# Kernel tuning notes

Measured on AMD Instinct MI355X. Metric: run time of the kernel, lower is better.

The kernel has to match this reference:

```python
import jax, jax.numpy as jnp
import numpy as np

B, C, N, M, K = 1, 64, 65536, 65536, 16
H, O = 64, 128  # mlp hidden, out_channels


def setup_inputs() -> dict:
    key = jax.random.key(0)
    ks = jax.random.split(key, 8)
    return {
        "x": jax.random.normal(ks[0], (B, C, N), dtype=jnp.float32),
        "pos": jax.random.normal(ks[1], (B, 3, N), dtype=jnp.float32),
        "support_points": jax.random.normal(ks[2], (B, 3, M), dtype=jnp.float32),
        "W1": jax.random.normal(ks[3], (H, C + 3), dtype=jnp.float32) * 0.05,
        "b1": jax.random.normal(ks[4], (H,), dtype=jnp.float32) * 0.05,
        "W2": jax.random.normal(ks[5], (O, H), dtype=jnp.float32) * 0.05,
        "b2": jax.random.normal(ks[6], (O,), dtype=jnp.float32) * 0.05,
        "indices": jax.random.randint(ks[7], (B, M, K), 0, N, dtype=jnp.int64),
    }


def _gather_points(t, indices):
    # t: [B, C, N], indices: [B, M, K] -> [B, C, M, K]
    b, c, n = t.shape
    m, k = indices.shape[1], indices.shape[2]
    idx = indices.reshape(b, 1, m * k)  # broadcasts over channel dim
    return jnp.take_along_axis(t, idx, axis=2).reshape(b, c, m, k)


def reference(x, pos, support_points, W1, b1, W2, b2, indices):
    # gather neighbor features and positions: [B, C, M, K], [B, 3, M, K]
    feats = _gather_points(x, indices)
    pts = _gather_points(pos, indices) - support_points[:, :, :, None]
    h = jnp.concatenate([feats, pts], axis=1)  # [B, C+3, M, K]
    # shared per-point MLP (1x1 Conv2d == channel contraction)
    h = jnp.einsum("oc,bcmk->bomk", W1, h) + b1[None, :, None, None]
    h = jax.nn.relu(h)
    h = jnp.einsum("oc,bcmk->bomk", W2, h) + b2[None, :, None, None]
    # max-pool over neighborhood K -> [B, O, M]
    return jnp.max(h, axis=3)
```

## Files before the change

### kernel.cpp

```cpp
#include <hip/hip_runtime.h>
#include <hip/hip_bf16.h>

#define NPTS 65536
#define MPTS 65536

typedef __attribute__((ext_vector_type(8))) short bf16x8;
typedef __attribute__((ext_vector_type(4))) float f32x4;

__device__ __forceinline__ float bflo(unsigned int u){ union{unsigned int i; float f;} v; v.i = u<<16; return v.f; }
__device__ __forceinline__ float bfhi(unsigned int u){ union{unsigned int i; float f;} v; v.i = u & 0xffff0000u; return v.f; }
__device__ __forceinline__ unsigned short f2bf(float f){
  union{float f; unsigned int i;} v; v.f=f;
  unsigned int r = v.i + 0x7fffu + ((v.i>>16)&1u);
  return (unsigned short)(r>>16);
}
__device__ __forceinline__ unsigned int pk2f(float a, float b){
  float2 tf; tf.x = a; tf.y = b;
  union { __hip_bfloat162 h; unsigned int u; } c;
  c.h = __float22bfloat162_rn(tf);
  return c.u;
}
__device__ __forceinline__ float swz16(float x){
  return __int_as_float(__builtin_amdgcn_ds_swizzle(__float_as_int(x), 0x401F));
}
__device__ __forceinline__ float red4(f32x4 a){
  return fmaxf(fmaxf(a[0], a[1]), fmaxf(a[2], a[3]));
}

#define MFMA32(a,b,c) __builtin_amdgcn_mfma_f32_16x16x32_bf16((a),(b),(c),0,0,0)

__global__ __launch_bounds__(256) void pack_all(
    const float* __restrict__ x,
    const float* __restrict__ pos,
    const float* __restrict__ sup,
    const float* __restrict__ W1,
    const float* __restrict__ b1,
    const float* __restrict__ W2,
    unsigned short* __restrict__ U,
    unsigned short* __restrict__ W2F,
    float* __restrict__ V) {
  const int t = threadIdx.x;
  if (blockIdx.x >= 1028) {
    const int m = (blockIdx.x - 1028) * 256 + t;
    const float s0 = sup[m], s1 = sup[MPTS + m], s2 = sup[2*MPTS + m];
    #pragma unroll
    for (int cg = 0; cg < 16; ++cg) {
      const float* r0 = W1 + (size_t)(cg*4 + 0)*67 + 64;
      const float* r1 = W1 + (size_t)(cg*4 + 1)*67 + 64;
      const float* r2 = W1 + (size_t)(cg*4 + 2)*67 + 64;
      const float* r3 = W1 + (size_t)(cg*4 + 3)*67 + 64;
      float4 o;
      o.x = r0[0]*s0 + r0[1]*s1 + r0[2]*s2;
      o.y = r1[0]*s0 + r1[1]*s1 + r1[2]*s2;
      o.z = r2[0]*s0 + r2[1]*s1 + r2[2]*s2;
      o.w = r3[0]*s0 + r3[1]*s1 + r3[2]*s2;
      *(float4*)(V + (size_t)m*64 + cg*4) = o;
    }
    return;
  }
  if (blockIdx.x >= 1024) {
    const int gg = (blockIdx.x - 1024) * 256 + t;
    if (gg < 1024) {
      const int g = gg >> 6, lane = gg & 63;
      const int q = lane >> 4, lr = lane & 15;
      const int kt = g >> 3, ot = g & 7;
      #pragma unroll
      for (int j = 0; j < 4; ++j)
        *(unsigned int*)&W2F[gg*8 + 2*j] =
            pk2f(W2[(ot*16 + lr)*64 + kt*32 + q*8 + 2*j],
                 W2[(ot*16 + lr)*64 + kt*32 + q*8 + 2*j + 1]);
    }
    return;
  }
  __shared__ float sx[67][65];
  const int n0 = blockIdx.x * 64;
  #pragma unroll
  for (int i = 0; i < 4; ++i) {
    const int lin = i*256 + t, r = lin >> 4, c4 = (lin & 15) * 4;
    const float4 v = *(const float4*)&x[(size_t)r * NPTS + n0 + c4];
    *(float4*)&sx[r][c4] = v;
  }
  if (t < 48) {
    const int lin = 1024 + t, r = lin >> 4, c4 = (lin & 15) * 4;
    const float4 v = *(const float4*)&pos[(size_t)(r - 64) * NPTS + n0 + c4];
    *(float4*)&sx[r][c4] = v;
  }

  const int lane = t & 63, w = t >> 6, quad = lane >> 4, lr = lane & 15;
  const int col = w * 16 + lr;
  const int n = n0 + col;

  bf16x8 wa[2][4], wt[4];
  #pragma unroll
  for (int kt = 0; kt < 2; ++kt)
    #pragma unroll
    for (int nt = 0; nt < 4; ++nt) {
      const float* r = W1 + (size_t)(nt*16 + lr)*67 + kt*32 + quad*8;
      const float4 a = *(const float4*)r;
      const float4 b = *(const float4*)(r + 4);
      union { unsigned int d[4]; bf16x8 v; } mk;
      mk.d[0] = pk2f(a.x, a.y); mk.d[1] = pk2f(a.z, a.w);
      mk.d[2] = pk2f(b.x, b.y); mk.d[3] = pk2f(b.z, b.w);
      wa[kt][nt] = mk.v;
    }
  #pragma unroll
  for (int nt = 0; nt < 4; ++nt) {
    union { unsigned int d[4]; bf16x8 v; } mk;
    mk.d[0] = 0u; mk.d[1] = 0u; mk.d[2] = 0u; mk.d[3] = 0u;
    if (quad == 0) {
      const float* r = W1 + (size_t)(nt*16 + lr)*67 + 64;
      mk.d[0] = pk2f(r[0], r[1]);
      mk.d[1] = (unsigned int)f2bf(r[2]);
    }
    wt[nt] = mk.v;
  }

  __syncthreads();

  const f32x4 fz = {0.f, 0.f, 0.f, 0.f};
  f32x4 acc[4] = {fz, fz, fz, fz};
  #pragma unroll
  for (int kt = 0; kt < 2; ++kt) {
    const int c0 = kt*32 + quad*8;
    union { unsigned int d[4]; bf16x8 v; } mk;
    #pragma unroll
    for (int i = 0; i < 4; ++i)
      mk.d[i] = pk2f(sx[c0 + 2*i][col], sx[c0 + 2*i + 1][col]);
    #pragma unroll
    for (int nt = 0; nt < 4; ++nt)
      acc[nt] = MFMA32(wa[kt][nt], mk.v, acc[nt]);
  }
  {
    union { unsigned int d[4]; bf16x8 v; } mk;
    mk.d[0] = pk2f(sx[64][col], sx[65][col]);
    mk.d[1] = (unsigned int)f2bf(sx[66][col]);
    mk.d[2] = 0u; mk.d[3] = 0u;
    #pragma unroll
    for (int nt = 0; nt < 4; ++nt)
      acc[nt] = MFMA32(wt[nt], mk.v, acc[nt]);
  }
  #pragma unroll
  for (int nt = 0; nt < 4; ++nt) {
    const float4 bb = *(const float4*)(b1 + nt*16 + quad*4);
    uint2 d;
    d.x = pk2f(acc[nt][0] + bb.x, acc[nt][1] + bb.y);
    d.y = pk2f(acc[nt][2] + bb.z, acc[nt][3] + bb.w);
    *(uint2*)(U + (size_t)n * 64 + nt*16 + quad*4) = d;
  }
}

__global__ __launch_bounds__(256, 3) void pointnet_reg7(
    const unsigned short* __restrict__ U,
    const float* __restrict__ V,
    const unsigned short* __restrict__ W2F,
    const float* __restrict__ b2,
    const int* __restrict__ indices,
    float* __restrict__ out) {
  __shared__ float sv[32][68];
  const int t = threadIdx.x;
  const int lane = t & 63, w = t >> 6, quad = lane >> 4, lr = lane & 15;
  const int mbase = blockIdx.x * 32;
  const int wbase = mbase + w * 8;

  const int vrow = w*8 + (lane >> 3), vcol = (lane & 7) * 8;
  const float* vg = &V[(size_t)(mbase + vrow) * 64 + vcol];
  const float4 va0 = *(const float4*)(vg);
  const float4 va1 = *(const float4*)(vg + 4);

  int idx0 = indices[(wbase + 0)*16 + lr];
  int idx1 = indices[(wbase + 1)*16 + lr];

  bf16x8 wf[16];
  #pragma unroll
  for (int k8 = 0; k8 < 16; ++k8) wf[k8] = ((const bf16x8*)W2F)[k8*64 + lane];

  *(float4*)&sv[vrow][vcol]     = va0;
  *(float4*)&sv[vrow][vcol + 4] = va1;

  uint4 urA0, urA1, urB0, urB1;
  { const size_t rb = (size_t)idx0 * 64;
    urA0 = *(const uint4*)(U + rb + quad*8);
    urA1 = *(const uint4*)(U + rb + 32 + quad*8); }

  float vstA[8], vstB[8];
  #pragma unroll
  for (int ot = 0; ot < 8; ++ot) { vstA[ot] = 0.f; vstB[ot] = 0.f; }

  const f32x4 fz = {0.f, 0.f, 0.f, 0.f};

#define PN_COMPUTE(PT, UR0, UR1)                                            \
  {                                                                         \
    const float* vr = &sv[w*8 + (PT)][quad*8];                              \
    const f32x4 v0 = *(const f32x4*)(vr);                                   \
    const f32x4 v1 = *(const f32x4*)(vr + 4);                               \
    const f32x4 v2 = *(const f32x4*)(vr + 32);                              \
    const f32x4 v3 = *(const f32x4*)(vr + 36);                              \
    const float vv[16] = {v0[0],v0[1],v0[2],v0[3], v1[0],v1[1],v1[2],v1[3], \
                          v2[0],v2[1],v2[2],v2[3], v3[0],v3[1],v3[2],v3[3]};\
    bf16x8 ah0, ah1;                                                        \
    {                                                                       \
      const unsigned int uu[4] = {(UR0).x,(UR0).y,(UR0).z,(UR0).w};         \
      union { unsigned int d[4]; bf16x8 v; } mk;                            \
      _Pragma("unroll")                                                     \
      for (int i = 0; i < 4; ++i) {                                         \
        const float lo = bflo(uu[i]) - vv[2*i];                             \
        const float hi = bfhi(uu[i]) - vv[2*i+1];                           \
        mk.d[i] = pk2f(fmaxf(lo, 0.f), fmaxf(hi, 0.f));                     \
      }                                                                     \
      ah0 = mk.v;                                                           \
    }                                                                       \
    {                                                                       \
      const unsigned int uu[4] = {(UR1).x,(UR1).y,(UR1).z,(UR1).w};         \
      union { unsigned int d[4]; bf16x8 v; } mk;                            \
      _Pragma("unroll")                                                     \
      for (int i = 0; i < 4; ++i) {                                         \
        const float lo = bflo(uu[i]) - vv[8+2*i];                           \
        const float hi = bfhi(uu[i]) - vv[8+2*i+1];                         \
        mk.d[i] = pk2f(fmaxf(lo, 0.f), fmaxf(hi, 0.f));                     \
      }                                                                     \
      ah1 = mk.v;                                                           \
    }                                                                       \
    const bool eA = ((PT) == 2*quad);                                       \
    const bool eB = ((PT) == 2*quad + 1);                                   \
    _Pragma("unroll")                                                       \
    for (int ot = 0; ot < 8; ++ot) {                                        \
      f32x4 a2 = MFMA32(ah0, wf[ot], fz);                                   \
      a2 = MFMA32(ah1, wf[8+ot], a2);                                       \
      float q = red4(a2);                                                   \
      q = fmaxf(q, swz16(q));                                               \
      q = fmaxf(q, __shfl_xor(q, 32));                                      \
      vstA[ot] = eA ? q : vstA[ot];                                         \
      vstB[ot] = eB ? q : vstB[ot];                                         \
    }                                                                       \
  }

  #pragma unroll 1
  for (int pp = 0; pp < 4; ++pp) {
    const int ptE = 2*pp, ptO = 2*pp + 1;
    { const size_t rb = (size_t)idx1 * 64;
      urB0 = *(const uint4*)(U + rb + quad*8);
      urB1 = *(const uint4*)(U + rb + 32 + quad*8); }
    { int nx = ptE + 2; nx = (nx > 7) ? 0 : nx;
      idx0 = indices[(wbase + nx)*16 + lr]; }
    PN_COMPUTE(ptE, urA0, urA1)
    { const size_t rb = (size_t)idx0 * 64;
      urA0 = *(const uint4*)(U + rb + quad*8);
      urA1 = *(const uint4*)(U + rb + 32 + quad*8); }
    { int nx = ptO + 2; nx = (nx > 7) ? 0 : nx;
      idx1 = indices[(wbase + nx)*16 + lr]; }
    PN_COMPUTE(ptO, urB0, urB1)
  }
#undef PN_COMPUTE

  #pragma unroll
  for (int ot = 0; ot < 8; ++ot) {
    const int o = ot*16 + lr;
    const float bb = b2[o];
    float2 st; st.x = vstA[ot] + bb; st.y = vstB[ot] + bb;
    *(float2*)&out[(size_t)o * MPTS + wbase + 2*quad] = st;
  }
}

__global__ __launch_bounds__(256, 3) void pointnet_reg(
    const unsigned short* __restrict__ U,
    const float* __restrict__ sup,
    const float* __restrict__ W1,
    const unsigned short* __restrict__ W2F,
    const float* __restrict__ b2,
    const int* __restrict__ indices,
    float* __restrict__ out) {
  const int t = threadIdx.x;
  const int lane = t & 63, w = t >> 6, quad = lane >> 4, lr = lane & 15;
  const int wbase = blockIdx.x * 32 + w * 8;

  int idx[8];
  #pragma unroll
  for (int pt = 0; pt < 8; ++pt) idx[pt] = indices[(wbase + pt)*16 + lr];

  uint4 ur[8][2];
  #pragma unroll
  for (int pt = 0; pt < 8; ++pt)
    #pragma unroll
    for (int kt = 0; kt < 2; ++kt)
      ur[pt][kt] = *(const uint4*)(U + (size_t)idx[pt]*64 + kt*32 + quad*8);

  bf16x8 ah[8][2];
  #pragma unroll
  for (int kt = 0; kt < 2; ++kt) {
    float w1p[8][3];
    #pragma unroll
    for (int j = 0; j < 8; ++j) {
      const float* r = W1 + (size_t)(kt*32 + quad*8 + j)*67 + 64;
      w1p[j][0] = r[0]; w1p[j][1] = r[1]; w1p[j][2] = r[2];
    }
    #pragma unroll
    for (int pt = 0; pt < 8; ++pt) {
      const float s0 = sup[wbase + pt];
      const float s1 = sup[MPTS + wbase + pt];
      const float s2 = sup[2*MPTS + wbase + pt];
      const unsigned int uu[4] = {ur[pt][kt].x, ur[pt][kt].y, ur[pt][kt].z, ur[pt][kt].w};
      union { unsigned int d[4]; bf16x8 v; } mk;
      #pragma unroll
      for (int i = 0; i < 4; ++i) {
        const float vl = w1p[2*i][0]*s0 + w1p[2*i][1]*s1 + w1p[2*i][2]*s2;
        const float vh = w1p[2*i+1][0]*s0 + w1p[2*i+1][1]*s1 + w1p[2*i+1][2]*s2;
        const float hl = fmaxf(bflo(uu[i]) - vl, 0.f);
        const float hh = fmaxf(bfhi(uu[i]) - vh, 0.f);
        mk.d[i] = pk2f(hl, hh);
      }
      ah[pt][kt] = mk.v;
    }
  }

  const f32x4 fz = {0.f, 0.f, 0.f, 0.f};
  #pragma unroll
  for (int ot = 0; ot < 8; ++ot) {
    const bf16x8 wb0 = ((const bf16x8*)W2F)[(0*8 + ot)*64 + lane];
    const bf16x8 wb1 = ((const bf16x8*)W2F)[(1*8 + ot)*64 + lane];
    float vm[8];
    #pragma unroll
    for (int pt = 0; pt < 8; ++pt) {
      f32x4 a2 = MFMA32(ah[pt][0], wb0, fz);
      a2 = MFMA32(ah[pt][1], wb1, a2);
      float v = fmaxf(fmaxf(a2[0], a2[1]), fmaxf(a2[2], a2[3]));
      v = fmaxf(v, __shfl_xor(v, 16));
      v = fmaxf(v, __shfl_xor(v, 32));
      vm[pt] = v;
    }
    const int o = ot*16 + lr;
    const float bb = b2[o];
    const float va = (quad & 1) ? ((quad & 2) ? vm[3] : vm[1])
                                : ((quad & 2) ? vm[2] : vm[0]);
    const float vb = (quad & 1) ? ((quad & 2) ? vm[7] : vm[5])
                                : ((quad & 2) ? vm[6] : vm[4]);
    out[(size_t)o * MPTS + wbase + quad] = va + bb;
    out[(size_t)o * MPTS + wbase + 4 + quad] = vb + bb;
  }
}

__global__ __launch_bounds__(256) void pointnet_fallback(
    const float* __restrict__ x, const float* __restrict__ pos,
    const float* __restrict__ sup,
    const float* __restrict__ W1, const float* __restrict__ b1,
    const float* __restrict__ W2, const float* __restrict__ b2,
    const int* __restrict__ indices, float* __restrict__ out) {
  __shared__ float sfeat[16][68];
  __shared__ float shid[16][64];
  __shared__ float smax[4][128];
  __shared__ int sidx[16];
  const int t = threadIdx.x;
  const int m = blockIdx.x;
  if (t < 16) sidx[t] = indices[m*16 + t];
  const float sup0 = sup[m], sup1 = sup[MPTS + m], sup2 = sup[2*MPTS + m];
  __syncthreads();
  for (int u = t; u < 16*17; u += 256) {
    const int k = u / 17, c4 = (u - k*17) * 4;
    const int idx = sidx[k];
    float4 wv;
    if (c4 < 64) {
      wv.x = x[(size_t)(c4+0)*NPTS + idx]; wv.y = x[(size_t)(c4+1)*NPTS + idx];
      wv.z = x[(size_t)(c4+2)*NPTS + idx]; wv.w = x[(size_t)(c4+3)*NPTS + idx];
    } else {
      wv.x = pos[idx] - sup0; wv.y = pos[NPTS + idx] - sup1;
      wv.z = pos[2*NPTS + idx] - sup2; wv.w = 0.f;
    }
    *(float4*)&sfeat[k][c4] = wv;
  }
  const int h = t & 63, kg = t >> 6;
  float w1r[68];
  #pragma unroll
  for (int c = 0; c < 67; ++c) w1r[c] = W1[h*67 + c];
  w1r[67] = 0.f;
  const float bias1 = b1[h];
  __syncthreads();
  #pragma unroll
  for (int j = 0; j < 4; ++j) {
    const int k = kg*4 + j;
    float a = bias1;
    const float4* rr = (const float4*)sfeat[k];
    #pragma unroll
    for (int qq = 0; qq < 17; ++qq) {
      const float4 v = rr[qq];
      a += w1r[qq*4+0]*v.x + w1r[qq*4+1]*v.y + w1r[qq*4+2]*v.z + w1r[qq*4+3]*v.w;
    }
    shid[k][h] = fmaxf(a, 0.f);
  }
  const int ow = t & 63;
  float w2a[64], w2b[64];
  #pragma unroll
  for (int hh = 0; hh < 64; ++hh) { w2a[hh] = W2[ow*64 + hh]; w2b[hh] = W2[(ow+64)*64 + hh]; }
  __syncthreads();
  float mxa = -3.0e38f, mxb = -3.0e38f;
  #pragma unroll
  for (int j = 0; j < 4; ++j) {
    const int k = kg*4 + j;
    const float4* hr = (const float4*)shid[k];
    float pa = 0.f, pb = 0.f;
    #pragma unroll
    for (int qq = 0; qq < 16; ++qq) {
      const float4 v = hr[qq];
      pa += w2a[qq*4+0]*v.x + w2a[qq*4+1]*v.y + w2a[qq*4+2]*v.z + w2a[qq*4+3]*v.w;
      pb += w2b[qq*4+0]*v.x + w2b[qq*4+1]*v.y + w2b[qq*4+2]*v.z + w2b[qq*4+3]*v.w;
    }
    mxa = fmaxf(mxa, pa); mxb = fmaxf(mxb, pb);
  }
  smax[kg][ow] = mxa; smax[kg][64 + ow] = mxb;
  __syncthreads();
  if (t < 128) {
    out[(size_t)t * MPTS + m] =
        fmaxf(fmaxf(smax[0][t], smax[1][t]), fmaxf(smax[2][t], smax[3][t])) + b2[t];
  }
}

extern "C" void kernel_launch(void* const* d_in, const int* in_sizes, int n_in,
                              void* d_out, int out_size, void* d_ws, size_t ws_size,
                              hipStream_t stream) {
  const float* x   = (const float*)d_in[0];
  const float* pos = (const float*)d_in[1];
  const float* sup = (const float*)d_in[2];
  const float* W1  = (const float*)d_in[3];
  const float* b1  = (const float*)d_in[4];
  const float* W2  = (const float*)d_in[5];
  const float* b2  = (const float*)d_in[6];
  const int* indices = (const int*)d_in[7];
  float* out = (float*)d_out;

  const size_t U_BYTES   = (size_t)NPTS * 64 * 2;
  const size_t W2F_BYTES = 16 * 64 * 8 * 2;
  const size_t V_BYTES   = (size_t)MPTS * 64 * 4;
  if (ws_size >= U_BYTES + W2F_BYTES + V_BYTES) {
    unsigned short* U   = (unsigned short*)d_ws;
    unsigned short* W2F = (unsigned short*)((char*)d_ws + U_BYTES);
    float* V            = (float*)((char*)d_ws + U_BYTES + W2F_BYTES);
    pack_all<<<1284, 256, 0, stream>>>(x, pos, sup, W1, b1, W2, U, W2F, V);
    pointnet_reg7<<<MPTS/32, 256, 0, stream>>>(U, V, W2F, b2, indices, out);
  } else if (ws_size >= U_BYTES + W2F_BYTES) {
    unsigned short* U   = (unsigned short*)d_ws;
    unsigned short* W2F = (unsigned short*)((char*)d_ws + U_BYTES);
    pack_all<<<1028, 256, 0, stream>>>(x, pos, sup, W1, b1, W2, U, W2F, nullptr);
    pointnet_reg<<<MPTS/32, 256, 0, stream>>>(U, sup, W1, W2F, b2, indices, out);
  } else {
    pointnet_fallback<<<MPTS, 256, 0, stream>>>(x, pos, sup, W1, b1, W2, b2, indices, out);
  }
}
```

Measured before the change: 136.2 us.

## Compute support-point W1 terms in main kernel and deepen neighbor gather prefetch

Drops the precomputed V buffer (16 MB of fp32 written by pack_all and read back by the main kernel). Each block now computes W1[:,64:67]·support_point directly into shared memory. The main loop now prefetches four neighbor rows at a time instead of two, and hoists the b2 bias loads. Launch bounds fall to 2 waves per SIMD to make room for the extra registers, which may reduce latency hiding. The unused pointnet_reg path is removed.

```diff
diff --git a/kernel.cpp b/kernel.cpp
--- a/kernel.cpp
+++ b/kernel.cpp
@@ -32,32 +32,12 @@
 __global__ __launch_bounds__(256) void pack_all(
     const float* __restrict__ x,
     const float* __restrict__ pos,
-    const float* __restrict__ sup,
     const float* __restrict__ W1,
     const float* __restrict__ b1,
     const float* __restrict__ W2,
     unsigned short* __restrict__ U,
-    unsigned short* __restrict__ W2F,
-    float* __restrict__ V) {
+    unsigned short* __restrict__ W2F) {
   const int t = threadIdx.x;
-  if (blockIdx.x >= 1028) {
-    const int m = (blockIdx.x - 1028) * 256 + t;
-    const float s0 = sup[m], s1 = sup[MPTS + m], s2 = sup[2*MPTS + m];
-    #pragma unroll
-    for (int cg = 0; cg < 16; ++cg) {
-      const float* r0 = W1 + (size_t)(cg*4 + 0)*67 + 64;
-      const float* r1 = W1 + (size_t)(cg*4 + 1)*67 + 64;
-      const float* r2 = W1 + (size_t)(cg*4 + 2)*67 + 64;
-      const float* r3 = W1 + (size_t)(cg*4 + 3)*67 + 64;
-      float4 o;
-      o.x = r0[0]*s0 + r0[1]*s1 + r0[2]*s2;
-      o.y = r1[0]*s0 + r1[1]*s1 + r1[2]*s2;
-      o.z = r2[0]*s0 + r2[1]*s1 + r2[2]*s2;
-      o.w = r3[0]*s0 + r3[1]*s1 + r3[2]*s2;
-      *(float4*)(V + (size_t)m*64 + cg*4) = o;
-    }
-    return;
-  }
   if (blockIdx.x >= 1024) {
     const int gg = (blockIdx.x - 1024) * 256 + t;
     if (gg < 1024) {
@@ -149,9 +129,10 @@
   }
 }
 
-__global__ __launch_bounds__(256, 3) void pointnet_reg7(
+__global__ __launch_bounds__(256, 2) void pointnet_reg8(
     const unsigned short* __restrict__ U,
-    const float* __restrict__ V,
+    const float* __restrict__ sup,
+    const float* __restrict__ W1,
     const unsigned short* __restrict__ W2F,
     const float* __restrict__ b2,
     const int* __restrict__ indices,
@@ -162,25 +143,47 @@
   const int mbase = blockIdx.x * 32;
   const int wbase = mbase + w * 8;
 
-  const int vrow = w*8 + (lane >> 3), vcol = (lane & 7) * 8;
-  const float* vg = &V[(size_t)(mbase + vrow) * 64 + vcol];
-  const float4 va0 = *(const float4*)(vg);
-  const float4 va1 = *(const float4*)(vg + 4);
-
   int idx0 = indices[(wbase + 0)*16 + lr];
   int idx1 = indices[(wbase + 1)*16 + lr];
-
-  bf16x8 wf[16];
-  #pragma unroll
-  for (int k8 = 0; k8 < 16; ++k8) wf[k8] = ((const bf16x8*)W2F)[k8*64 + lane];
-
-  *(float4*)&sv[vrow][vcol]     = va0;
-  *(float4*)&sv[vrow][vcol + 4] = va1;
-
-  uint4 urA0, urA1, urB0, urB1;
+  int idx2 = indices[(wbase + 2)*16 + lr];
+  int idx3 = indices[(wbase + 3)*16 + lr];
+
+  const int vrow = w*8 + (lane >> 3), vcol = (lane & 7) * 8;
+  const int m = mbase + vrow;
+  const float s0 = sup[m], s1 = sup[MPTS + m], s2 = sup[2*MPTS + m];
+  float vvv[8];
+  #pragma unroll
+  for (int j = 0; j < 8; ++j) {
+    const float* r = W1 + (size_t)(vcol + j)*67 + 64;
+    vvv[j] = r[0]*s0 + r[1]*s1 + r[2]*s2;
+  }
+  { float4 o0, o1;
+    o0.x = vvv[0]; o0.y = vvv[1]; o0.z = vvv[2]; o0.w = vvv[3];
+    o1.x = vvv[4]; o1.y = vvv[5]; o1.z = vvv[6]; o1.w = vvv[7];
+    *(float4*)&sv[vrow][vcol]     = o0;
+    *(float4*)&sv[vrow][vcol + 4] = o1; }
+
+  uint4 urA0, urA1, urB0, urB1, urC0, urC1, urD0, urD1;
   { const size_t rb = (size_t)idx0 * 64;
     urA0 = *(const uint4*)(U + rb + quad*8);
     urA1 = *(const uint4*)(U + rb + 32 + quad*8); }
+  { const size_t rb = (size_t)idx1 * 64;
+    urB0 = *(const uint4*)(U + rb + quad*8);
+    urB1 = *(const uint4*)(U + rb + 32 + quad*8); }
+  { const size_t rb = (size_t)idx2 * 64;
+    urC0 = *(const uint4*)(U + rb + quad*8);
+    urC1 = *(const uint4*)(U + rb + 32 + quad*8); }
+  { const size_t rb = (size_t)idx3 * 64;
+    urD0 = *(const uint4*)(U + rb + quad*8);
+    urD1 = *(const uint4*)(U + rb + 32 + quad*8); }
+
+  bf16x8 wf[16];
+  #pragma unroll
+  for (int k8 = 0; k8 < 16; ++k8) wf[k8] = ((const bf16x8*)W2F)[k8*64 + lane];
+
+  float bias[8];
+  #pragma unroll
+  for (int ot = 0; ot < 8; ++ot) bias[ot] = b2[ot*16 + lr];
 
   float vstA[8], vstB[8];
   #pragma unroll
@@ -235,106 +238,38 @@
   }
 
   #pragma unroll 1
-  for (int pp = 0; pp < 4; ++pp) {
-    const int ptE = 2*pp, ptO = 2*pp + 1;
-    { const size_t rb = (size_t)idx1 * 64;
+  for (int pp = 0; pp < 2; ++pp) {
+    const int base = 4*pp;
+    if (pp == 0) {
+      idx0 = indices[(wbase + 4)*16 + lr];
+      idx1 = indices[(wbase + 5)*16 + lr];
+      idx2 = indices[(wbase + 6)*16 + lr];
+      idx3 = indices[(wbase + 7)*16 + lr];
+    }
+    PN_COMPUTE(base + 0, urA0, urA1)
+    if (pp == 0) { const size_t rb = (size_t)idx0 * 64;
+      urA0 = *(const uint4*)(U + rb + quad*8);
+      urA1 = *(const uint4*)(U + rb + 32 + quad*8); }
+    PN_COMPUTE(base + 1, urB0, urB1)
+    if (pp == 0) { const size_t rb = (size_t)idx1 * 64;
       urB0 = *(const uint4*)(U + rb + quad*8);
       urB1 = *(const uint4*)(U + rb + 32 + quad*8); }
-    { int nx = ptE + 2; nx = (nx > 7) ? 0 : nx;
-      idx0 = indices[(wbase + nx)*16 + lr]; }
-    PN_COMPUTE(ptE, urA0, urA1)
-    { const size_t rb = (size_t)idx0 * 64;
-      urA0 = *(const uint4*)(U + rb + quad*8);
-      urA1 = *(const uint4*)(U + rb + 32 + quad*8); }
-    { int nx = ptO + 2; nx = (nx > 7) ? 0 : nx;
-      idx1 = indices[(wbase + nx)*16 + lr]; }
-    PN_COMPUTE(ptO, urB0, urB1)
+    PN_COMPUTE(base + 2, urC0, urC1)
+    if (pp == 0) { const size_t rb = (size_t)idx2 * 64;
+      urC0 = *(const uint4*)(U + rb + quad*8);
+      urC1 = *(const uint4*)(U + rb + 32 + quad*8); }
+    PN_COMPUTE(base + 3, urD0, urD1)
+    if (pp == 0) { const size_t rb = (size_t)idx3 * 64;
+      urD0 = *(const uint4*)(U + rb + quad*8);
+      urD1 = *(const uint4*)(U + rb + 32 + quad*8); }
   }
 #undef PN_COMPUTE
 
   #pragma unroll
   for (int ot = 0; ot < 8; ++ot) {
     const int o = ot*16 + lr;
-    const float bb = b2[o];
-    float2 st; st.x = vstA[ot] + bb; st.y = vstB[ot] + bb;
+    float2 st; st.x = vstA[ot] + bias[ot]; st.y = vstB[ot] + bias[ot];
     *(float2*)&out[(size_t)o * MPTS + wbase + 2*quad] = st;
-  }
-}
-
-__global__ __launch_bounds__(256, 3) void pointnet_reg(
-    const unsigned short* __restrict__ U,
-    const float* __restrict__ sup,
-    const float* __restrict__ W1,
-    const unsigned short* __restrict__ W2F,
-    const float* __restrict__ b2,
-    const int* __restrict__ indices,
-    float* __restrict__ out) {
-  const int t = threadIdx.x;
-  const int lane = t & 63, w = t >> 6, quad = lane >> 4, lr = lane & 15;
-  const int wbase = blockIdx.x * 32 + w * 8;
-
-  int idx[8];
-  #pragma unroll
-  for (int pt = 0; pt < 8; ++pt) idx[pt] = indices[(wbase + pt)*16 + lr];
-
-  uint4 ur[8][2];
-  #pragma unroll
-  for (int pt = 0; pt < 8; ++pt)
-    #pragma unroll
-    for (int kt = 0; kt < 2; ++kt)
-      ur[pt][kt] = *(const uint4*)(U + (size_t)idx[pt]*64 + kt*32 + quad*8);
-
-  bf16x8 ah[8][2];
-  #pragma unroll
-  for (int kt = 0; kt < 2; ++kt) {
-    float w1p[8][3];
-    #pragma unroll
-    for (int j = 0; j < 8; ++j) {
-      const float* r = W1 + (size_t)(kt*32 + quad*8 + j)*67 + 64;
-      w1p[j][0] = r[0]; w1p[j][1] = r[1]; w1p[j][2] = r[2];
-    }
-    #pragma unroll
-    for (int pt = 0; pt < 8; ++pt) {
-      const float s0 = sup[wbase + pt];
-      const float s1 = sup[MPTS + wbase + pt];
-      const float s2 = sup[2*MPTS + wbase + pt];
-      const unsigned int uu[4] = {ur[pt][kt].x, ur[pt][kt].y, ur[pt][kt].z, ur[pt][kt].w};
-      union { unsigned int d[4]; bf16x8 v; } mk;
-      #pragma unroll
-      for (int i = 0; i < 4; ++i) {
-        const float vl = w1p[2*i][0]*s0 + w1p[2*i][1]*s1 + w1p[2*i][2]*s2;
-        const float vh = w1p[2*i+1][0]*s0 + w1p[2*i+1][1]*s1 + w1p[2*i+1][2]*s2;
-        const float hl = fmaxf(bflo(uu[i]) - vl, 0.f);
-        const float hh = fmaxf(bfhi(uu[i]) - vh, 0.f);
-        mk.d[i] = pk2f(hl, hh);
-      }
-      ah[pt][kt] = mk.v;
-    }
-  }
-
-  const f32x4 fz = {0.f, 0.f, 0.f, 0.f};
-  #pragma unroll
-  for (int ot = 0; ot < 8; ++ot) {
-    const bf16x8 wb0 = ((const bf16x8*)W2F)[(0*8 + ot)*64 + lane];
-    const bf16x8 wb1 = ((const bf16x8*)W2F)[(1*8 + ot)*64 + lane];
-    float vm[8];
-    #pragma unroll
-    for (int pt = 0; pt < 8; ++pt) {
-      f32x4 a2 = MFMA32(ah[pt][0], wb0, fz);
-      a2 = MFMA32(ah[pt][1], wb1, a2);
-      float v = fmaxf(fmaxf(a2[0], a2[1]), fmaxf(a2[2], a2[3]));
-      v = fmaxf(v, __shfl_xor(v, 16));
-      v = fmaxf(v, __shfl_xor(v, 32));
-      vm[pt] = v;
-    }
-    const int o = ot*16 + lr;
-    const float bb = b2[o];
-    const float va = (quad & 1) ? ((quad & 2) ? vm[3] : vm[1])
-                                : ((quad & 2) ? vm[2] : vm[0]);
-    const float vb = (quad & 1) ? ((quad & 2) ? vm[7] : vm[5])
-                                : ((quad & 2) ? vm[6] : vm[4]);
-    out[(size_t)o * MPTS + wbase + quad] = va + bb;
-    out[(size_t)o * MPTS + wbase + 4 + quad] = vb + bb;
   }
 }
 
@@ -427,18 +362,11 @@
 
   const size_t U_BYTES   = (size_t)NPTS * 64 * 2;
   const size_t W2F_BYTES = 16 * 64 * 8 * 2;
-  const size_t V_BYTES   = (size_t)MPTS * 64 * 4;
-  if (ws_size >= U_BYTES + W2F_BYTES + V_BYTES) {
+  if (ws_size >= U_BYTES + W2F_BYTES) {
     unsigned short* U   = (unsigned short*)d_ws;
     unsigned short* W2F = (unsigned short*)((char*)d_ws + U_BYTES);
-    float* V            = (float*)((char*)d_ws + U_BYTES + W2F_BYTES);
-    pack_all<<<1284, 256, 0, stream>>>(x, pos, sup, W1, b1, W2, U, W2F, V);
-    pointnet_reg7<<<MPTS/32, 256, 0, stream>>>(U, V, W2F, b2, indices, out);
-  } else if (ws_size >= U_BYTES + W2F_BYTES) {
-    unsigned short* U   = (unsigned short*)d_ws;
-    unsigned short* W2F = (unsigned short*)((char*)d_ws + U_BYTES);
-    pack_all<<<1028, 256, 0, stream>>>(x, pos, sup, W1, b1, W2, U, W2F, nullptr);
-    pointnet_reg<<<MPTS/32, 256, 0, stream>>>(U, sup, W1, W2F, b2, indices, out);
+    pack_all<<<1028, 256, 0, stream>>>(x, pos, W1, b1, W2, U, W2F);
+    pointnet_reg8<<<MPTS/32, 256, 0, stream>>>(U, sup, W1, W2F, b2, indices, out);
   } else {
     pointnet_fallback<<<MPTS, 256, 0, stream>>>(x, pos, sup, W1, b1, W2, b2, indices, out);
   }
```

New measurement: 138.6 us. Within noise of the previous version (+1.8%).
